# Kernel optimization log

Hardware: AMD Instinct MI355X
Metric: run time of the kernel (lower is better)

Reference implementation:

```python
import jax, jax.numpy as jnp
import numpy as np

DT = 0.1
THRESH = 10.0

def setup_inputs() -> dict:
    key = jax.random.key(0)
    ks = jax.random.split(key, 6)
    B, S, H, V = 2, 1024, 1024, 50257
    hidden_states = jax.random.normal(ks[0], (B, S, H), dtype=jnp.float32)
    ttu_state = jnp.zeros((B, 3), dtype=jnp.float32)
    W_imp = jax.random.normal(ks[1], (3, H), dtype=jnp.float32) * 0.02
    b_imp = jnp.zeros((3,), dtype=jnp.float32)
    W_lm = jax.random.normal(ks[2], (V, H), dtype=jnp.float32) * 0.02
    W_mod = jax.random.normal(ks[3], (V, 3), dtype=jnp.float32) * 0.02
    # gamma, alpha_c, beta_c, delta, alpha_d, epsilon, alpha_m
    ttu_params = jax.random.uniform(ks[4], (7,), dtype=jnp.float32, minval=0.1, maxval=1.0)
    return {"hidden_states": hidden_states, "ttu_state": ttu_state,
            "W_imp": W_imp, "b_imp": b_imp, "W_lm": W_lm, "W_mod": W_mod,
            "ttu_params": ttu_params}

def _ttu_scan(ttu_state, impulses, ttu_params):
    # impulses: [S, B, 3] (time-major for scan)
    gamma, alpha_c, beta_c, delta, alpha_d, epsilon, alpha_m = ttu_params
    def step(state, imp):
        phi_c, phi_d, phi_m = state[:, 0], state[:, 1], state[:, 2]
        dphi_c = gamma * imp[:, 0] - alpha_c * phi_c - beta_c * phi_c * phi_d
        dphi_d = delta * phi_c ** 2 - alpha_d * phi_d
        dphi_m = epsilon * phi_d - alpha_m * phi_m
        new_c = phi_c + DT * dphi_c
        new_d = phi_d + DT * dphi_d
        new_m = phi_m + DT * dphi_m
        # saturation damping on phi_d
        new_d = jnp.where(jnp.abs(new_d) > THRESH, jnp.float32(0.5), jnp.float32(1.0)) * new_d
        new_state = jnp.stack([new_c, new_d, new_m], axis=1)  # [B, 3]
        return new_state, new_state
    return jax.lax.scan(step, ttu_state, impulses)

def reference(hidden_states, ttu_state, W_imp, b_imp, W_lm, W_mod, ttu_params):
    # impulse projections computed in batch up front: [S, B, 3]
    impulses = jnp.einsum('bsh,dh->sbd', hidden_states, W_imp) + b_imp
    final_state, states = _ttu_scan(ttu_state, impulses, ttu_params)  # states: [S, B, 3]
    # base lm logits + 0.1 * modulation from ttu trajectory
    logits = jnp.einsum('bsh,vh->bsv', hidden_states, W_lm) \
           + 0.1 * jnp.einsum('sbd,vd->bsv', states, W_mod)
    return logits, final_state
```

## Files before the change

### kernel.cpp

```cpp
#include <hip/hip_runtime.h>
#include <hip/hip_bf16.h>

typedef float  f32x4  __attribute__((ext_vector_type(4)));
typedef short  bf16x8 __attribute__((ext_vector_type(8)));
typedef short  bf16x4 __attribute__((ext_vector_type(4)));

typedef const void __attribute__((address_space(1))) gv_t;
typedef void __attribute__((address_space(3))) sv_t;

namespace {

constexpr int B_ = 2;
constexpr int S_ = 1024;
constexpr int H_ = 1024;
constexpr int V_ = 50257;
constexpr int M_ = B_ * S_;
constexpr int VP_ = 50304;
constexpr float DT_ = 0.1f;
constexpr float THRESH_ = 10.0f;

constexpr int BM = 128, BN = 128, BK = 64;
constexpr int NT = H_ / BK;

__device__ __forceinline__ unsigned short f2bf(float f) {
  union { float f; unsigned u; } x;
  x.f = f;
  x.u += 0x7FFFu + ((x.u >> 16) & 1u);
  return (unsigned short)(x.u >> 16);
}

__global__ void cvt_hidden_impulse_kernel(const float* __restrict__ hidden,
                                          const float* __restrict__ W_imp,
                                          const float* __restrict__ b_imp,
                                          unsigned short* __restrict__ hid_bf,
                                          float* __restrict__ imp) {
  const int m = blockIdx.x;
  const int t = threadIdx.x;
  const float4 hv = reinterpret_cast<const float4*>(hidden + (size_t)m * H_)[t];
  const float4 wv = reinterpret_cast<const float4*>(W_imp)[t];
  bf16x4 o;
  o[0] = (short)f2bf(hv.x); o[1] = (short)f2bf(hv.y);
  o[2] = (short)f2bf(hv.z); o[3] = (short)f2bf(hv.w);
  *(bf16x4*)(hid_bf + (size_t)m * H_ + t * 4) = o;
  float p = hv.x * wv.x + hv.y * wv.y + hv.z * wv.z + hv.w * wv.w;
  #pragma unroll
  for (int off = 32; off; off >>= 1) p += __shfl_down(p, off);
  __shared__ float partial[4];
  if ((t & 63) == 0) partial[t >> 6] = p;
  __syncthreads();
  if (t == 0) {
    const float v = partial[0] + partial[1] + partial[2] + partial[3] + b_imp[0];
    const int b = m >> 10;
    const int s = m & (S_ - 1);
    imp[s * B_ + b] = v;
  }
}

__global__ void ttu_scan_kernel(const float* __restrict__ imp,
                                const float* __restrict__ ttu_state,
                                const float* __restrict__ ttu_params,
                                float* __restrict__ states,
                                float* __restrict__ final_out) {
  __shared__ float imp_s[S_ * B_];
  const int t = threadIdx.x;
  for (int i = t; i < S_ * B_; i += 64) imp_s[i] = imp[i];
  __syncthreads();
  if (t < B_) {
    const float gamma   = ttu_params[0];
    const float alpha_c = ttu_params[1];
    const float beta_c  = ttu_params[2];
    const float delta   = ttu_params[3];
    const float alpha_d = ttu_params[4];
    const float epsilon = ttu_params[5];
    const float alpha_m = ttu_params[6];
    float c = ttu_state[t * 3 + 0];
    float d = ttu_state[t * 3 + 1];
    float m = ttu_state[t * 3 + 2];
    for (int s = 0; s < S_; ++s) {
      const float ii = imp_s[s * B_ + t];
      const float dc = gamma * ii - alpha_c * c - beta_c * c * d;
      const float dd = delta * c * c - alpha_d * d;
      const float dm = epsilon * d - alpha_m * m;
      c = c + DT_ * dc;
      float nd = d + DT_ * dd;
      m = m + DT_ * dm;
      nd = (fabsf(nd) > THRESH_ ? 0.5f : 1.0f) * nd;
      d = nd;
      float* st = states + (size_t)(s * B_ + t) * 3;
      st[0] = c; st[1] = d; st[2] = m;
    }
    final_out[t * 3 + 0] = c;
    final_out[t * 3 + 1] = d;
    final_out[t * 3 + 2] = m;
  }
}

__global__ void cvt_bf16_kernel(const float* __restrict__ src,
                                unsigned short* __restrict__ dst,
                                long n_src, long n_dst) {
  const long stride = (long)gridDim.x * blockDim.x * 8;
  for (long i = ((long)blockIdx.x * blockDim.x + threadIdx.x) * 8; i < n_dst; i += stride) {
    bf16x8 v;
    if (i < n_src) {
      const float4 a = *(const float4*)(src + i);
      const float4 b = *(const float4*)(src + i + 4);
      v[0] = (short)f2bf(a.x); v[1] = (short)f2bf(a.y);
      v[2] = (short)f2bf(a.z); v[3] = (short)f2bf(a.w);
      v[4] = (short)f2bf(b.x); v[5] = (short)f2bf(b.y);
      v[6] = (short)f2bf(b.z); v[7] = (short)f2bf(b.w);
    } else {
      v = (bf16x8){0, 0, 0, 0, 0, 0, 0, 0};
    }
    *(bf16x8*)(dst + i) = v;
  }
}

__global__ __launch_bounds__(256) void ttu_gemm_bf16_db_kernel(
    const unsigned short* __restrict__ Ab,
    const unsigned short* __restrict__ Bb,
    const float* __restrict__ states,
    const float* __restrict__ Wmod,
    float* __restrict__ out)
{
  __shared__ unsigned short AB_s[2][2][BM * BK];
  __shared__ float st_s[BM][3];
  __shared__ float wm_s[BN][3];

  const int t = threadIdx.x;
  const int cpx = gridDim.x >> 3;
  const int bid = (blockIdx.x & 7) * cpx + (blockIdx.x >> 3);
  const int mb = bid & 15;
  const int nb = bid >> 4;
  const int m0 = mb * BM;
  const int n0 = nb * BN;

  if (t < BM) {
    const int m = m0 + t;
    const int b = m >> 10;
    const int s = m & (S_ - 1);
    const float* st = states + (size_t)(s * B_ + b) * 3;
    st_s[t][0] = st[0]; st_s[t][1] = st[1]; st_s[t][2] = st[2];
  } else {
    const int tt = t - BM;
    const int n = n0 + tt;
    const bool ok = n < V_;
    wm_s[tt][0] = ok ? Wmod[n * 3 + 0] : 0.f;
    wm_s[tt][1] = ok ? Wmod[n * 3 + 1] : 0.f;
    wm_s[tt][2] = ok ? Wmod[n * 3 + 2] : 0.f;
  }

  const int lane = t & 63;
  const int wid  = t >> 6;
  const int lr   = lane >> 3;
  const int ch   = lane & 7;
  const int wm   = wid >> 1;
  const int wn   = wid & 1;
  const int lm   = lane & 15;
  const int kg   = lane >> 4;

  const unsigned short* Abase = Ab + (size_t)m0 * H_;
  const unsigned short* Bbase = Bb + (size_t)n0 * H_;

  const int r0 = wid * 32;
  auto STAGE = [&](unsigned short* As, unsigned short* Bs, int kt) {
    const int k0 = kt * BK;
    #pragma unroll
    for (int ins = 0; ins < 4; ++ins) {
      const int lrow = r0 + ins * 8 + lr;
      const int sch  = ch ^ (lrow & 7);
      __builtin_amdgcn_global_load_lds(
          (gv_t*)(Abase + (size_t)lrow * H_ + k0 + sch * 8),
          (sv_t*)(As + (r0 + ins * 8) * BK), 16, 0, 0);
    }
    #pragma unroll
    for (int ins = 0; ins < 4; ++ins) {
      const int lrow = r0 + ins * 8 + lr;
      const int sch  = ch ^ (lrow & 7);
      __builtin_amdgcn_global_load_lds(
          (gv_t*)(Bbase + (size_t)lrow * H_ + k0 + sch * 8),
          (sv_t*)(Bs + (r0 + ins * 8) * BK), 16, 0, 0);
    }
  };

  f32x4 acc[4][4];
  #pragma unroll
  for (int i = 0; i < 4; ++i)
    #pragma unroll
    for (int j = 0; j < 4; ++j)
      acc[i][j] = (f32x4){0.f, 0.f, 0.f, 0.f};

  unsigned short* Ac = &AB_s[0][0][0];
  unsigned short* Bc = &AB_s[0][1][0];
  unsigned short* An = &AB_s[1][0][0];
  unsigned short* Bn = &AB_s[1][1][0];

  STAGE(Ac, Bc, 0);
  __syncthreads();

  for (int kt = 0; kt < NT; ++kt) {
    if (kt + 1 < NT) STAGE(An, Bn, kt + 1);

    bf16x8 af[4][2], bfr[4][2];
    #pragma unroll
    for (int i = 0; i < 4; ++i) {
      const int arow = wm * 64 + i * 16 + lm;
      const int brow = wn * 64 + i * 16 + lm;
      #pragma unroll
      for (int ks = 0; ks < 2; ++ks) {
        af[i][ks]  = *(const bf16x8*)&Ac[arow * BK + (((ks * 4 + kg) ^ (arow & 7)) << 3)];
        bfr[i][ks] = *(const bf16x8*)&Bc[brow * BK + (((ks * 4 + kg) ^ (brow & 7)) << 3)];
      }
    }
    #pragma unroll
    for (int ks = 0; ks < 2; ++ks)
      #pragma unroll
      for (int i = 0; i < 4; ++i)
        #pragma unroll
        for (int j = 0; j < 4; ++j)
          acc[i][j] = __builtin_amdgcn_mfma_f32_16x16x32_bf16(af[i][ks], bfr[j][ks], acc[i][j], 0, 0, 0);

    __syncthreads();
    unsigned short* tp;
    tp = Ac; Ac = An; An = tp;
    tp = Bc; Bc = Bn; Bn = tp;
  }

  #pragma unroll
  for (int i = 0; i < 4; ++i) {
    #pragma unroll
    for (int rr = 0; rr < 4; ++rr) {
      const int mloc = wm * 64 + i * 16 + kg * 4 + rr;
      const float s0 = st_s[mloc][0], s1 = st_s[mloc][1], s2 = st_s[mloc][2];
      float* orow = out + (size_t)(m0 + mloc) * V_ + n0;
      #pragma unroll
      for (int j = 0; j < 4; ++j) {
        const int nloc = wn * 64 + j * 16 + lm;
        if (n0 + nloc < V_) {
          const float corr = 0.1f * (s0 * wm_s[nloc][0] + s1 * wm_s[nloc][1] + s2 * wm_s[nloc][2]);
          orow[nloc] = acc[i][j][rr] + corr;
        }
      }
    }
  }
}

__global__ __launch_bounds__(256) void ttu_gemm_kernel(
    const float* __restrict__ Ag, const float* __restrict__ Bg,
    const float* __restrict__ states, const float* __restrict__ Wmod,
    float* __restrict__ out)
{
  __shared__ unsigned short A_s[BM][40];
  __shared__ unsigned short B_s[BM][40];
  __shared__ float st_s[BM][3];
  __shared__ float wm_s[BM][3];

  const int t   = threadIdx.x;
  const int bid = blockIdx.x;
  const int mb  = bid & 15;
  const int nb  = bid >> 4;
  const int m0  = mb * BM;
  const int n0  = nb * BM;

  if (t < BM) {
    const int m = m0 + t;
    const int b = m >> 10;
    const int s = m & (S_ - 1);
    const float* st = states + (size_t)(s * B_ + b) * 3;
    st_s[t][0] = st[0]; st_s[t][1] = st[1]; st_s[t][2] = st[2];
  } else {
    const int tt = t - BM;
    const int n  = n0 + tt;
    const bool ok = n < V_;
    wm_s[tt][0] = ok ? Wmod[n * 3 + 0] : 0.f;
    wm_s[tt][1] = ok ? Wmod[n * 3 + 1] : 0.f;
    wm_s[tt][2] = ok ? Wmod[n * 3 + 2] : 0.f;
  }

  const int r   = t >> 1;
  const int seg = t & 1;
  const float* arow = Ag + (size_t)(m0 + r) * H_ + seg * 16;
  const int  vrow = n0 + r;
  const bool bok  = vrow < V_;
  const float* brow = Bg + (size_t)(bok ? vrow : 0) * H_ + seg * 16;

  const int lane = t & 63;
  const int wid  = t >> 6;
  const int wm   = wid >> 1;
  const int wn   = wid & 1;
  const int lm   = lane & 15;
  const int kg   = lane >> 4;

  f32x4 acc[4][4];
  #pragma unroll
  for (int i = 0; i < 4; ++i)
    #pragma unroll
    for (int j = 0; j < 4; ++j)
      acc[i][j] = (f32x4){0.f, 0.f, 0.f, 0.f};

  for (int kt = 0; kt < H_ / 32; ++kt) {
    const int k0 = kt * 32;
    const float4 av0 = *(const float4*)(arow + k0 + 0);
    const float4 av1 = *(const float4*)(arow + k0 + 4);
    const float4 av2 = *(const float4*)(arow + k0 + 8);
    const float4 av3 = *(const float4*)(arow + k0 + 12);
    float4 bv0 = {0,0,0,0}, bv1 = {0,0,0,0}, bv2 = {0,0,0,0}, bv3 = {0,0,0,0};
    if (bok) {
      bv0 = *(const float4*)(brow + k0 + 0);
      bv1 = *(const float4*)(brow + k0 + 4);
      bv2 = *(const float4*)(brow + k0 + 8);
      bv3 = *(const float4*)(brow + k0 + 12);
    }
    __syncthreads();
    #define CVT4(v) (bf16x4){(short)f2bf((v).x), (short)f2bf((v).y), (short)f2bf((v).z), (short)f2bf((v).w)}
    *(bf16x4*)&A_s[r][seg * 16 + 0]  = CVT4(av0);
    *(bf16x4*)&A_s[r][seg * 16 + 4]  = CVT4(av1);
    *(bf16x4*)&A_s[r][seg * 16 + 8]  = CVT4(av2);
    *(bf16x4*)&A_s[r][seg * 16 + 12] = CVT4(av3);
    *(bf16x4*)&B_s[r][seg * 16 + 0]  = CVT4(bv0);
    *(bf16x4*)&B_s[r][seg * 16 + 4]  = CVT4(bv1);
    *(bf16x4*)&B_s[r][seg * 16 + 8]  = CVT4(bv2);
    *(bf16x4*)&B_s[r][seg * 16 + 12] = CVT4(bv3);
    #undef CVT4
    __syncthreads();
    bf16x8 af[4], bf[4];
    #pragma unroll
    for (int i = 0; i < 4; ++i) {
      af[i] = *(const bf16x8*)&A_s[wm * 64 + i * 16 + lm][kg * 8];
      bf[i] = *(const bf16x8*)&B_s[wn * 64 + i * 16 + lm][kg * 8];
    }
    #pragma unroll
    for (int i = 0; i < 4; ++i)
      #pragma unroll
      for (int j = 0; j < 4; ++j)
        acc[i][j] = __builtin_amdgcn_mfma_f32_16x16x32_bf16(af[i], bf[j], acc[i][j], 0, 0, 0);
  }

  #pragma unroll
  for (int i = 0; i < 4; ++i) {
    #pragma unroll
    for (int rr = 0; rr < 4; ++rr) {
      const int mloc = wm * 64 + i * 16 + kg * 4 + rr;
      const float s0 = st_s[mloc][0], s1 = st_s[mloc][1], s2 = st_s[mloc][2];
      float* orow = out + (size_t)(m0 + mloc) * V_ + n0;
      #pragma unroll
      for (int j = 0; j < 4; ++j) {
        const int nloc = wn * 64 + j * 16 + lm;
        if (n0 + nloc < V_) {
          const float corr = 0.1f * (s0 * wm_s[nloc][0] + s1 * wm_s[nloc][1] + s2 * wm_s[nloc][2]);
          orow[nloc] = acc[i][j][rr] + corr;
        }
      }
    }
  }
}

}

extern "C" void kernel_launch(void* const* d_in, const int* in_sizes, int n_in,
                              void* d_out, int out_size, void* d_ws, size_t ws_size,
                              hipStream_t stream) {
  const float* hidden     = (const float*)d_in[0];
  const float* ttu_state  = (const float*)d_in[1];
  const float* W_imp      = (const float*)d_in[2];
  const float* b_imp      = (const float*)d_in[3];
  const float* W_lm       = (const float*)d_in[4];
  const float* W_mod      = (const float*)d_in[5];
  const float* ttu_params = (const float*)d_in[6];
  float* out = (float*)d_out;

  float* imp    = (float*)d_ws;
  float* states = imp + S_ * B_;

  const size_t need = 32768 + (size_t)M_ * H_ * 2 + (size_t)VP_ * H_ * 2;
  const int grid = (VP_ / BN) * (M_ / BM);

  if (ws_size >= need) {
    unsigned short* hid_bf = (unsigned short*)((char*)d_ws + 32768);
    unsigned short* wlm_bf = hid_bf + (size_t)M_ * H_;
    cvt_hidden_impulse_kernel<<<M_, 256, 0, stream>>>(hidden, W_imp, b_imp, hid_bf, imp);
    ttu_scan_kernel<<<1, 64, 0, stream>>>(imp, ttu_state, ttu_params, states,
                                          out + (size_t)B_ * S_ * V_);
    cvt_bf16_kernel<<<4096, 256, 0, stream>>>(W_lm, wlm_bf,
                                              (long)V_ * H_, (long)VP_ * H_);
    ttu_gemm_bf16_db_kernel<<<grid, 256, 0, stream>>>(hid_bf, wlm_bf, states, W_mod, out);
  } else {
    cvt_hidden_impulse_kernel<<<M_, 256, 0, stream>>>(hidden, W_imp, b_imp,
                                                      (unsigned short*)d_ws , imp);
    ttu_scan_kernel<<<1, 64, 0, stream>>>(imp, ttu_state, ttu_params, states,
                                          out + (size_t)B_ * S_ * V_);
    ttu_gemm_kernel<<<grid, 256, 0, stream>>>(hidden, W_lm, states, W_mod, out);
  }
}
```

Before: 525.2 us.

## Add 256x256-tile pipelined bf16 GEMM and fold TTU scan into weight conversion

Adds a new GEMM kernel with 256x256 output tiles, 512 threads and 8 waves, and double-buffered LDS. Loads for the next k-tile are split into four quarter stages that are interleaved with MFMA groups, and the MFMA sections run at raised wave priority. The serial TTU scan now runs in an extra block of the W_lm bf16 conversion kernel, so one launch is dropped and the scan overlaps the conversion. The larger tiles halve global re-reads of the operands but use much more LDS and registers. The vocabulary is padded to a multiple of 256, which needs a larger workspace, and the old 128-tile path is kept as a fallback.

After: 550.8 us. 1.05x slower.

```diff
diff --git a/kernel.cpp b/kernel.cpp
--- a/kernel.cpp
+++ b/kernel.cpp
@@ -15,11 +15,12 @@
 constexpr int H_ = 1024;
 constexpr int V_ = 50257;
 constexpr int M_ = B_ * S_;
-constexpr int VP_ = 50304;
+constexpr int VP2_ = 50432;
+constexpr int VP1_ = 50304;
 constexpr float DT_ = 0.1f;
 constexpr float THRESH_ = 10.0f;
 
-constexpr int BM = 128, BN = 128, BK = 64;
+constexpr int BK = 64;
 constexpr int NT = H_ / BK;
 
 __device__ __forceinline__ unsigned short f2bf(float f) {
@@ -56,15 +57,11 @@
   }
 }
 
-__global__ void ttu_scan_kernel(const float* __restrict__ imp,
-                                const float* __restrict__ ttu_state,
-                                const float* __restrict__ ttu_params,
-                                float* __restrict__ states,
-                                float* __restrict__ final_out) {
-  __shared__ float imp_s[S_ * B_];
-  const int t = threadIdx.x;
-  for (int i = t; i < S_ * B_; i += 64) imp_s[i] = imp[i];
-  __syncthreads();
+__device__ __forceinline__ void scan_body(const float* __restrict__ imp_s,
+                                          const float* __restrict__ ttu_state,
+                                          const float* __restrict__ ttu_params,
+                                          float* __restrict__ states,
+                                          float* __restrict__ final_out, int t) {
   if (t < B_) {
     const float gamma   = ttu_params[0];
     const float alpha_c = ttu_params[1];
@@ -95,6 +92,51 @@
   }
 }
 
+__global__ void ttu_scan_kernel(const float* __restrict__ imp,
+                                const float* __restrict__ ttu_state,
+                                const float* __restrict__ ttu_params,
+                                float* __restrict__ states,
+                                float* __restrict__ final_out) {
+  __shared__ float imp_s[S_ * B_];
+  const int t = threadIdx.x;
+  for (int i = t; i < S_ * B_; i += 64) imp_s[i] = imp[i];
+  __syncthreads();
+  scan_body(imp_s, ttu_state, ttu_params, states, final_out, t);
+}
+
+__global__ void cvt_wlm_scan_kernel(const float* __restrict__ src,
+                                    unsigned short* __restrict__ dst,
+                                    long n_src, long n_dst,
+                                    const float* __restrict__ imp,
+                                    const float* __restrict__ ttu_state,
+                                    const float* __restrict__ ttu_params,
+                                    float* __restrict__ states,
+                                    float* __restrict__ final_out) {
+  __shared__ float imp_s[S_ * B_];
+  const int t = threadIdx.x;
+  if (blockIdx.x == gridDim.x - 1) {
+    for (int i = t; i < S_ * B_; i += 256) imp_s[i] = imp[i];
+    __syncthreads();
+    scan_body(imp_s, ttu_state, ttu_params, states, final_out, t);
+    return;
+  }
+  const long stride = (long)(gridDim.x - 1) * blockDim.x * 8;
+  for (long i = ((long)blockIdx.x * blockDim.x + t) * 8; i < n_dst; i += stride) {
+    bf16x8 v;
+    if (i < n_src) {
+      const float4 a = *(const float4*)(src + i);
+      const float4 b = *(const float4*)(src + i + 4);
+      v[0] = (short)f2bf(a.x); v[1] = (short)f2bf(a.y);
+      v[2] = (short)f2bf(a.z); v[3] = (short)f2bf(a.w);
+      v[4] = (short)f2bf(b.x); v[5] = (short)f2bf(b.y);
+      v[6] = (short)f2bf(b.z); v[7] = (short)f2bf(b.w);
+    } else {
+      v = (bf16x8){0, 0, 0, 0, 0, 0, 0, 0};
+    }
+    *(bf16x8*)(dst + i) = v;
+  }
+}
+
 __global__ void cvt_bf16_kernel(const float* __restrict__ src,
                                 unsigned short* __restrict__ dst,
                                 long n_src, long n_dst) {
@@ -115,6 +157,158 @@
   }
 }
 
+__global__ __launch_bounds__(512, 2) void ttu_gemm_bf16_256_kernel(
+    const unsigned short* __restrict__ Ab,
+    const unsigned short* __restrict__ Bb,
+    const float* __restrict__ states,
+    const float* __restrict__ Wmod,
+    float* __restrict__ out)
+{
+  __shared__ unsigned short A_s[2][256 * BK];
+  __shared__ unsigned short B_s[2][256 * BK];
+  __shared__ float st_s[256][3];
+  __shared__ float wm_s[256][3];
+
+  const int t = threadIdx.x;
+  const int cpx = gridDim.x >> 3;
+  const int bid = (blockIdx.x & 7) * cpx + (blockIdx.x >> 3);
+  const int mb = bid & 7;
+  const int nb = bid >> 3;
+  const int m0 = mb * 256;
+  const int n0 = nb * 256;
+
+  if (t < 256) {
+    const int m = m0 + t;
+    const int b = m >> 10;
+    const int s = m & (S_ - 1);
+    const float* st = states + (size_t)(s * B_ + b) * 3;
+    st_s[t][0] = st[0]; st_s[t][1] = st[1]; st_s[t][2] = st[2];
+  } else {
+    const int tt = t - 256;
+    const int n = n0 + tt;
+    const bool ok = n < V_;
+    wm_s[tt][0] = ok ? Wmod[n * 3 + 0] : 0.f;
+    wm_s[tt][1] = ok ? Wmod[n * 3 + 1] : 0.f;
+    wm_s[tt][2] = ok ? Wmod[n * 3 + 2] : 0.f;
+  }
+
+  const int lane = t & 63;
+  const int wid  = t >> 6;
+  const int lr   = lane >> 3;
+  const int ch   = lane & 7;
+  const int wmi  = wid >> 2;
+  const int wni  = wid & 3;
+  const int lm   = lane & 15;
+  const int kg   = lane >> 4;
+
+  const unsigned short* Abase = Ab + (size_t)m0 * H_;
+  const unsigned short* Bbase = Bb + (size_t)n0 * H_;
+
+  auto STAGE_HALF = [&](int buf, int kt, int h) {
+    const int k0 = kt * BK;
+    const unsigned short* gb = (h < 2) ? Abase : Bbase;
+    unsigned short* ls = (h < 2) ? &A_s[buf][0] : &B_s[buf][0];
+    const int half = (h & 1) * 128;
+    #pragma unroll
+    for (int n = 0; n < 2; ++n) {
+      const int rbase = half + wid * 16 + n * 8;
+      const int r  = rbase + lr;
+      const int sc = ch ^ (r & 7);
+      __builtin_amdgcn_global_load_lds(
+          (gv_t*)(gb + (size_t)r * H_ + k0 + sc * 8),
+          (sv_t*)(ls + rbase * BK), 16, 0, 0);
+    }
+  };
+
+  f32x4 acc[8][4];
+  #pragma unroll
+  for (int i = 0; i < 8; ++i)
+    #pragma unroll
+    for (int j = 0; j < 4; ++j)
+      acc[i][j] = (f32x4){0.f, 0.f, 0.f, 0.f};
+
+  #pragma unroll
+  for (int h = 0; h < 4; ++h) STAGE_HALF(0, 0, h);
+  asm volatile("s_waitcnt vmcnt(0)" ::: "memory");
+  __builtin_amdgcn_s_barrier();
+  __builtin_amdgcn_sched_barrier(0);
+
+  int cur = 0;
+  bf16x8 bfr[4][2];
+
+  for (int kt = 0; kt < NT; ++kt) {
+    const int nxt = cur ^ 1;
+    const bool more = (kt + 1 < NT);
+    const unsigned short* As = &A_s[cur][0];
+    const unsigned short* Bs = &B_s[cur][0];
+
+    if (more) {
+      STAGE_HALF(nxt, kt + 1, 0);
+      asm volatile("s_waitcnt vmcnt(2)" ::: "memory");
+    } else {
+      asm volatile("s_waitcnt vmcnt(0)" ::: "memory");
+    }
+    __builtin_amdgcn_s_barrier();
+    __builtin_amdgcn_sched_barrier(0);
+
+    #pragma unroll
+    for (int q = 0; q < 4; ++q) {
+      if (q > 0 && more) STAGE_HALF(nxt, kt + 1, q);
+      if (q == 0) {
+        #pragma unroll
+        for (int j = 0; j < 4; ++j)
+          #pragma unroll
+          for (int ks = 0; ks < 2; ++ks) {
+            const int r = wni * 64 + j * 16 + lm;
+            bfr[j][ks] = *(const bf16x8*)&Bs[r * BK + (((ks * 4 + kg) ^ (r & 7)) << 3)];
+          }
+      }
+      bf16x8 af[2][2];
+      #pragma unroll
+      for (int i2 = 0; i2 < 2; ++i2)
+        #pragma unroll
+        for (int ks = 0; ks < 2; ++ks) {
+          const int r = wmi * 128 + (q * 2 + i2) * 16 + lm;
+          af[i2][ks] = *(const bf16x8*)&As[r * BK + (((ks * 4 + kg) ^ (r & 7)) << 3)];
+        }
+      asm volatile("s_waitcnt lgkmcnt(0)" ::: "memory");
+      __builtin_amdgcn_sched_barrier(0);
+      __builtin_amdgcn_s_setprio(1);
+      #pragma unroll
+      for (int ks = 0; ks < 2; ++ks)
+        #pragma unroll
+        for (int i2 = 0; i2 < 2; ++i2)
+          #pragma unroll
+          for (int j = 0; j < 4; ++j)
+            acc[q * 2 + i2][j] = __builtin_amdgcn_mfma_f32_16x16x32_bf16(
+                af[i2][ks], bfr[j][ks], acc[q * 2 + i2][j], 0, 0, 0);
+      __builtin_amdgcn_s_setprio(0);
+    }
+
+    __builtin_amdgcn_s_barrier();
+    __builtin_amdgcn_sched_barrier(0);
+    cur ^= 1;
+  }
+
+  #pragma unroll
+  for (int i = 0; i < 8; ++i) {
+    #pragma unroll
+    for (int rr = 0; rr < 4; ++rr) {
+      const int mloc = wmi * 128 + i * 16 + kg * 4 + rr;
+      const float s0 = st_s[mloc][0], s1 = st_s[mloc][1], s2 = st_s[mloc][2];
+      float* orow = out + (size_t)(m0 + mloc) * V_ + n0;
+      #pragma unroll
+      for (int j = 0; j < 4; ++j) {
+        const int nloc = wni * 64 + j * 16 + lm;
+        if (n0 + nloc < V_) {
+          const float corr = 0.1f * (s0 * wm_s[nloc][0] + s1 * wm_s[nloc][1] + s2 * wm_s[nloc][2]);
+          orow[nloc] = acc[i][j][rr] + corr;
+        }
+      }
+    }
+  }
+}
+
 __global__ __launch_bounds__(256) void ttu_gemm_bf16_db_kernel(
     const unsigned short* __restrict__ Ab,
     const unsigned short* __restrict__ Bb,
@@ -122,26 +316,26 @@
     const float* __restrict__ Wmod,
     float* __restrict__ out)
 {
-  __shared__ unsigned short AB_s[2][2][BM * BK];
-  __shared__ float st_s[BM][3];
-  __shared__ float wm_s[BN][3];
+  __shared__ unsigned short AB_s[2][2][128 * BK];
+  __shared__ float st_s[128][3];
+  __shared__ float wm_s[128][3];
 
   const int t = threadIdx.x;
   const int cpx = gridDim.x >> 3;
   const int bid = (blockIdx.x & 7) * cpx + (blockIdx.x >> 3);
   const int mb = bid & 15;
   const int nb = bid >> 4;
-  const int m0 = mb * BM;
-  const int n0 = nb * BN;
-
-  if (t < BM) {
+  const int m0 = mb * 128;
+  const int n0 = nb * 128;
+
+  if (t < 128) {
     const int m = m0 + t;
     const int b = m >> 10;
     const int s = m & (S_ - 1);
     const float* st = states + (size_t)(s * B_ + b) * 3;
     st_s[t][0] = st[0]; st_s[t][1] = st[1]; st_s[t][2] = st[2];
   } else {
-    const int tt = t - BM;
+    const int tt = t - 128;
     const int n = n0 + tt;
     const bool ok = n < V_;
     wm_s[tt][0] = ok ? Wmod[n * 3 + 0] : 0.f;
@@ -160,8 +354,8 @@
 
   const unsigned short* Abase = Ab + (size_t)m0 * H_;
   const unsigned short* Bbase = Bb + (size_t)n0 * H_;
-
   const int r0 = wid * 32;
+
   auto STAGE = [&](unsigned short* As, unsigned short* Bs, int kt) {
     const int k0 = kt * BK;
     #pragma unroll
@@ -199,7 +393,6 @@
 
   for (int kt = 0; kt < NT; ++kt) {
     if (kt + 1 < NT) STAGE(An, Bn, kt + 1);
-
     bf16x8 af[4][2], bfr[4][2];
     #pragma unroll
     for (int i = 0; i < 4; ++i) {
@@ -218,7 +411,6 @@
         #pragma unroll
         for (int j = 0; j < 4; ++j)
           acc[i][j] = __builtin_amdgcn_mfma_f32_16x16x32_bf16(af[i][ks], bfr[j][ks], acc[i][j], 0, 0, 0);
-
     __syncthreads();
     unsigned short* tp;
     tp = Ac; Ac = An; An = tp;
@@ -249,26 +441,26 @@
     const float* __restrict__ states, const float* __restrict__ Wmod,
     float* __restrict__ out)
 {
-  __shared__ unsigned short A_s[BM][40];
-  __shared__ unsigned short B_s[BM][40];
-  __shared__ float st_s[BM][3];
-  __shared__ float wm_s[BM][3];
+  __shared__ unsigned short A_s[128][40];
+  __shared__ unsigned short B_s[128][40];
+  __shared__ float st_s[128][3];
+  __shared__ float wm_s[128][3];
 
   const int t   = threadIdx.x;
   const int bid = blockIdx.x;
   const int mb  = bid & 15;
   const int nb  = bid >> 4;
-  const int m0  = mb * BM;
-  const int n0  = nb * BM;
-
-  if (t < BM) {
+  const int m0  = mb * 128;
+  const int n0  = nb * 128;
+
+  if (t < 128) {
     const int m = m0 + t;
     const int b = m >> 10;
     const int s = m & (S_ - 1);
     const float* st = states + (size_t)(s * B_ + b) * 3;
     st_s[t][0] = st[0]; st_s[t][1] = st[1]; st_s[t][2] = st[2];
   } else {
-    const int tt = t - BM;
+    const int tt = t - 128;
     const int n  = n0 + tt;
     const bool ok = n < V_;
     wm_s[tt][0] = ok ? Wmod[n * 3 + 0] : 0.f;
@@ -370,24 +562,34 @@
 
   float* imp    = (float*)d_ws;
   float* states = imp + S_ * B_;
-
-  const size_t need = 32768 + (size_t)M_ * H_ * 2 + (size_t)VP_ * H_ * 2;
-  const int grid = (VP_ / BN) * (M_ / BM);
-
-  if (ws_size >= need) {
+  float* final_out = out + (size_t)B_ * S_ * V_;
+
+  const size_t need256 = 32768 + (size_t)M_ * H_ * 2 + (size_t)VP2_ * H_ * 2;
+  const size_t need128 = 32768 + (size_t)M_ * H_ * 2 + (size_t)VP1_ * H_ * 2;
+
+  if (ws_size >= need256) {
     unsigned short* hid_bf = (unsigned short*)((char*)d_ws + 32768);
     unsigned short* wlm_bf = hid_bf + (size_t)M_ * H_;
     cvt_hidden_impulse_kernel<<<M_, 256, 0, stream>>>(hidden, W_imp, b_imp, hid_bf, imp);
-    ttu_scan_kernel<<<1, 64, 0, stream>>>(imp, ttu_state, ttu_params, states,
-                                          out + (size_t)B_ * S_ * V_);
-    cvt_bf16_kernel<<<4096, 256, 0, stream>>>(W_lm, wlm_bf,
-                                              (long)V_ * H_, (long)VP_ * H_);
+    cvt_wlm_scan_kernel<<<4097, 256, 0, stream>>>(W_lm, wlm_bf,
+                                                  (long)V_ * H_, (long)VP2_ * H_,
+                                                  imp, ttu_state, ttu_params,
+                                                  states, final_out);
+    const int grid = (VP2_ / 256) * (M_ / 256);
+    ttu_gemm_bf16_256_kernel<<<grid, 512, 0, stream>>>(hid_bf, wlm_bf, states, W_mod, out);
+  } else if (ws_size >= need128) {
+    unsigned short* hid_bf = (unsigned short*)((char*)d_ws + 32768);
+    unsigned short* wlm_bf = hid_bf + (size_t)M_ * H_;
+    cvt_hidden_impulse_kernel<<<M_, 256, 0, stream>>>(hidden, W_imp, b_imp, hid_bf, imp);
+    ttu_scan_kernel<<<1, 64, 0, stream>>>(imp, ttu_state, ttu_params, states, final_out);
+    cvt_bf16_kernel<<<4096, 256, 0, stream>>>(W_lm, wlm_bf, (long)V_ * H_, (long)VP1_ * H_);
+    const int grid = (VP1_ / 128) * (M_ / 128);
     ttu_gemm_bf16_db_kernel<<<grid, 256, 0, stream>>>(hid_bf, wlm_bf, states, W_mod, out);
   } else {
     cvt_hidden_impulse_kernel<<<M_, 256, 0, stream>>>(hidden, W_imp, b_imp,
-                                                      (unsigned short*)d_ws , imp);
-    ttu_scan_kernel<<<1, 64, 0, stream>>>(imp, ttu_state, ttu_params, states,
-                                          out + (size_t)B_ * S_ * V_);
+                                                      (unsigned short*)d_ws, imp);
+    ttu_scan_kernel<<<1, 64, 0, stream>>>(imp, ttu_state, ttu_params, states, final_out);
+    const int grid = ((V_ + 127) / 128) * (M_ / 128);
     ttu_gemm_kernel<<<grid, 256, 0, stream>>>(hidden, W_lm, states, W_mod, out);
   }
 }
```
